# Performance work log

Hardware: AMD Instinct MI355X
Metric: run time of the kernel (lower is better)

Reference implementation:

```python
import jax, jax.numpy as jnp
import numpy as np

B, T, C, V = 8, 2048, 1024, 32000


def setup_inputs() -> dict:
    key = jax.random.key(0)
    ks = jax.random.split(key, 12)
    s = 1.0 / np.sqrt(C)
    return {
        "input_tokens": jax.random.randint(ks[0], (B, T), 0, V),
        "xx_init": jnp.zeros((B, C), jnp.float32),
        "aa_init": jnp.zeros((B, C), jnp.float32),
        "bb_init": jnp.zeros((B, C), jnp.float32),
        "pp_init": jnp.zeros((B, C), jnp.float32),  # with aa=bb=0 this is equivalent to -inf init
        "emb": jax.random.normal(ks[1], (V, C), jnp.float32) * 0.02,
        "time_mix_k": jax.random.uniform(ks[2], (C,), jnp.float32),
        "time_mix_v": jax.random.uniform(ks[3], (C,), jnp.float32),
        "time_mix_r": jax.random.uniform(ks[4], (C,), jnp.float32),
        "time_decay": jax.random.normal(ks[5], (C,), jnp.float32) * 0.1,
        "time_first": jax.random.normal(ks[6], (C,), jnp.float32) * 0.1,
        "Wk": jax.random.normal(ks[7], (C, C), jnp.float32) * s,
        "Wv": jax.random.normal(ks[8], (C, C), jnp.float32) * s,
        "Wr": jax.random.normal(ks[9], (C, C), jnp.float32) * s,
        "Wo": jax.random.normal(ks[10], (C, C), jnp.float32) * s,
    }


def _wkv_scan(k, v, aa0, bb0, pp0, w, u):
    """Numerically-stable RWKV WKV recurrence.
    k, v: [T, B, C]; aa0/bb0/pp0: [B, C]; w (decay, negative), u (bonus): [C]."""
    def step(carry, kv):
        aa, bb, pp = carry
        kt, vt = kv
        ww = u + kt
        p = jnp.maximum(pp, ww)
        e1 = jnp.exp(pp - p)
        e2 = jnp.exp(ww - p)
        wkv = (e1 * aa + e2 * vt) / (e1 * bb + e2)
        ww2 = pp + w
        p2 = jnp.maximum(ww2, kt)
        e1b = jnp.exp(ww2 - p2)
        e2b = jnp.exp(kt - p2)
        return (e1b * aa + e2b * vt, e1b * bb + e2b, p2), wkv
    (aa, bb, pp), out = jax.lax.scan(step, (aa0, bb0, pp0), (k, v))
    return out, aa, bb, pp


def _forward(input_tokens, xx_init, aa_init, bb_init, pp_init, emb,
             time_mix_k, time_mix_v, time_mix_r, time_decay, time_first,
             Wk, Wv, Wr, Wo):
    x = emb[input_tokens]                                   # [B, T, C]
    xprev = jnp.concatenate([xx_init[:, None, :], x[:, :-1]], axis=1)  # token shift
    xk = x * time_mix_k + xprev * (1.0 - time_mix_k)
    xv = x * time_mix_v + xprev * (1.0 - time_mix_v)
    xr = x * time_mix_r + xprev * (1.0 - time_mix_r)
    k = jnp.einsum("btc,dc->btd", xk, Wk)
    v = jnp.einsum("btc,dc->btd", xv, Wv)
    r = jax.nn.sigmoid(jnp.einsum("btc,dc->btd", xr, Wr))
    w = -jnp.exp(time_decay)                                # per-channel decay
    u = time_first
    wkv, _, _, _ = _wkv_scan(jnp.swapaxes(k, 0, 1), jnp.swapaxes(v, 0, 1),
                             aa_init, bb_init, pp_init, w, u)
    wkv = jnp.swapaxes(wkv, 0, 1)                           # [B, T, C]
    rwkv = jnp.einsum("btc,dc->btd", r * wkv, Wo)
    e1 = rwkv[:, -1]          # final-step state
    e2 = rwkv.mean(axis=1)    # time-averaged state
    hx = (e1 + e2) * 0.5
    return jnp.stack([hx, hx])  # (hx, cx) stacked -> [2, B, C]


def reference(input_tokens, xx_init, aa_init, bb_init, pp_init, emb,
              time_mix_k, time_mix_v, time_mix_r, time_decay, time_first,
              Wk, Wv, Wr, Wo):
    return _forward(input_tokens, xx_init, aa_init, bb_init, pp_init, emb,
                    time_mix_k, time_mix_v, time_mix_r, time_decay, time_first,
                    Wk, Wv, Wr, Wo)
```

## Files before the change

kernel.cpp:

```cpp
#include <hip/hip_runtime.h>

#define Bdim 8
#define Tdim 2048
#define Cdim 1024
#define CHUNK 128
#define NCHUNK 16
#define BC (Bdim*Cdim)

typedef float floatx4 __attribute__((ext_vector_type(4)));
typedef _Float16 half8 __attribute__((ext_vector_type(8)));
typedef _Float16 half4v __attribute__((ext_vector_type(4)));

__device__ __forceinline__ void load16(const void* g, void* l) {
    __builtin_amdgcn_global_load_lds(
        (const __attribute__((address_space(1))) void*)g,
        (__attribute__((address_space(3))) void*)l, 16, 0, 0);
}

__global__ __launch_bounds__(256) void embed_mix(const int* __restrict__ tokens,
                                                 const float* __restrict__ xx_init,
                                                 const float* __restrict__ emb,
                                                 _Float16* __restrict__ xe) {
    int row = blockIdx.x;
    int b = row / (Tdim + 1);
    int tt = row % (Tdim + 1);
    const float* src;
    if (tt == 0) src = xx_init + (size_t)b * Cdim;
    else         src = emb + (size_t)tokens[b * Tdim + tt - 1] * Cdim;
    int c0 = threadIdx.x * 4;
    float4 f = *reinterpret_cast<const float4*>(src + c0);
    half4v h;
    h[0] = (_Float16)f.x; h[1] = (_Float16)f.y; h[2] = (_Float16)f.z; h[3] = (_Float16)f.w;
    *reinterpret_cast<half4v*>(xe + (size_t)row * Cdim + c0) = h;
}

__global__ __launch_bounds__(256) void mix3(const _Float16* __restrict__ xe,
                                            const float* __restrict__ tmk,
                                            const float* __restrict__ tmv,
                                            const float* __restrict__ tmr,
                                            _Float16* __restrict__ xk,
                                            _Float16* __restrict__ xv,
                                            _Float16* __restrict__ xr) {
    int row = blockIdx.x;
    int b = row >> 11;
    int t = row & (Tdim - 1);
    const _Float16* cur = xe + ((size_t)(b * (Tdim + 1) + t + 1)) * Cdim;
    const _Float16* prv = cur - Cdim;
    int c = threadIdx.x * 4;
    half4v cu = *reinterpret_cast<const half4v*>(cur + c);
    half4v pv = *reinterpret_cast<const half4v*>(prv + c);
    float4 mk = *reinterpret_cast<const float4*>(tmk + c);
    float4 mv = *reinterpret_cast<const float4*>(tmv + c);
    float4 mr = *reinterpret_cast<const float4*>(tmr + c);
    half4v hk, hv, hr;
    float cf[4] = {(float)cu[0], (float)cu[1], (float)cu[2], (float)cu[3]};
    float pf[4] = {(float)pv[0], (float)pv[1], (float)pv[2], (float)pv[3]};
    float mkf[4] = {mk.x, mk.y, mk.z, mk.w};
    float mvf[4] = {mv.x, mv.y, mv.z, mv.w};
    float mrf[4] = {mr.x, mr.y, mr.z, mr.w};
    #pragma unroll
    for (int j = 0; j < 4; j++) {
        hk[j] = (_Float16)(mkf[j] * cf[j] + (1.0f - mkf[j]) * pf[j]);
        hv[j] = (_Float16)(mvf[j] * cf[j] + (1.0f - mvf[j]) * pf[j]);
        hr[j] = (_Float16)(mrf[j] * cf[j] + (1.0f - mrf[j]) * pf[j]);
    }
    size_t o = (size_t)row * Cdim + c;
    *reinterpret_cast<half4v*>(xk + o) = hk;
    *reinterpret_cast<half4v*>(xv + o) = hv;
    *reinterpret_cast<half4v*>(xr + o) = hr;
}

__global__ __launch_bounds__(256) void wconv(const float* __restrict__ Wk,
                                             const float* __restrict__ Wv,
                                             const float* __restrict__ Wr,
                                             _Float16* __restrict__ Wh) {
    const float* W = blockIdx.y == 0 ? Wk : (blockIdx.y == 1 ? Wv : Wr);
    _Float16* dst = Wh + (size_t)blockIdx.y * Cdim * Cdim;
    int i = (blockIdx.x * 256 + threadIdx.x) * 4;
    float4 f = *reinterpret_cast<const float4*>(W + i);
    half4v h;
    h[0] = (_Float16)f.x; h[1] = (_Float16)f.y; h[2] = (_Float16)f.z; h[3] = (_Float16)f.w;
    *reinterpret_cast<half4v*>(dst + i) = h;
}

__global__ __launch_bounds__(512, 2) void gemm_kvr(const _Float16* __restrict__ xk,
                                                   const _Float16* __restrict__ xv,
                                                   const _Float16* __restrict__ xr,
                                                   const _Float16* __restrict__ Wh,
                                                   _Float16* __restrict__ ko,
                                                   _Float16* __restrict__ vo,
                                                   _Float16* __restrict__ ro) {
    const int which = blockIdx.y;
    const _Float16* X = which == 0 ? xk : (which == 1 ? xv : xr);
    const _Float16* W = Wh + (size_t)which * Cdim * Cdim;
    _Float16* out     = which == 0 ? ko : (which == 1 ? vo : ro);

    const int lin = blockIdx.x;
    const int xcd = lin & 7;
    const int loc = lin >> 3;
    const int mt = xcd * 8 + (loc >> 2);
    const int nt = loc & 3;
    const int m0 = mt * 256;
    const int n0 = nt * 256;

    __shared__ _Float16 As[4 * 8192];
    __shared__ _Float16 Bs[4 * 8192];

    const int tid = threadIdx.x;
    const int lane = tid & 63;
    const int wave = tid >> 6;
    const int wm = (wave >> 2) * 128;
    const int wn = (wave & 3) * 64;
    const int lr = lane & 15;
    const int lk = lane >> 4;
    const int sw = (lr >> 1) & 3;

    const _Float16* Asrc = X + (size_t)m0 * Cdim;
    const _Float16* Bsrc = W + (size_t)n0 * Cdim;

    floatx4 acc[8][4] = {};

    auto stageA = [&](int kt) {
        const int p = kt & 3;
        const int k0 = kt * 32;
        #pragma unroll
        for (int i = 0; i < 2; i++) {
            int e = i * 512 + tid;
            int r = e >> 2;
            int cp = e & 3;
            int cl = cp ^ ((r >> 1) & 3);
            load16(Asrc + (size_t)r * Cdim + k0 + cl * 8, (char*)(As + p * 8192) + e * 16);
        }
    };
    auto stageB = [&](int kt) {
        const int p = kt & 3;
        const int k0 = kt * 32;
        #pragma unroll
        for (int i = 0; i < 2; i++) {
            int e = i * 512 + tid;
            int r = e >> 2;
            int cp = e & 3;
            int cl = cp ^ ((r >> 1) & 3);
            load16(Bsrc + (size_t)r * Cdim + k0 + cl * 8, (char*)(Bs + p * 8192) + e * 16);
        }
    };

    auto ktile = [&](int kt, bool st) {
        const int p = kt & 3;
        const _Float16* ap = As + p * 8192 + (wm + lr) * 32 + (lk ^ sw) * 8;
        const _Float16* bp = Bs + p * 8192 + (wn + lr) * 32 + (lk ^ sw) * 8;
        half8 af[8], bf[4];
        #pragma unroll
        for (int mi = 0; mi < 4; mi++)
            af[mi] = *reinterpret_cast<const half8*>(ap + mi * 512);
        #pragma unroll
        for (int ni = 0; ni < 4; ni++)
            bf[ni] = *reinterpret_cast<const half8*>(bp + ni * 512);
        if (st) stageA(kt + 3);
        __builtin_amdgcn_s_barrier();
        asm volatile("s_waitcnt lgkmcnt(0)" ::: "memory");
        __builtin_amdgcn_sched_barrier(0);
        __builtin_amdgcn_s_setprio(1);
        #pragma unroll
        for (int mi = 0; mi < 4; mi++)
            #pragma unroll
            for (int ni = 0; ni < 4; ni++)
                acc[mi][ni] = __builtin_amdgcn_mfma_f32_16x16x32_f16(af[mi], bf[ni], acc[mi][ni], 0, 0, 0);
        __builtin_amdgcn_s_setprio(0);
        __builtin_amdgcn_sched_barrier(0);
        __builtin_amdgcn_s_barrier();
        #pragma unroll
        for (int mi = 4; mi < 8; mi++)
            af[mi] = *reinterpret_cast<const half8*>(ap + mi * 512);
        if (st) stageB(kt + 3);
        __builtin_amdgcn_s_barrier();
        asm volatile("s_waitcnt lgkmcnt(0)" ::: "memory");
        __builtin_amdgcn_sched_barrier(0);
        __builtin_amdgcn_s_setprio(1);
        #pragma unroll
        for (int mi = 4; mi < 8; mi++)
            #pragma unroll
            for (int ni = 0; ni < 4; ni++)
                acc[mi][ni] = __builtin_amdgcn_mfma_f32_16x16x32_f16(af[mi], bf[ni], acc[mi][ni], 0, 0, 0);
        __builtin_amdgcn_s_setprio(0);
        __builtin_amdgcn_sched_barrier(0);
    };

    stageA(0); stageB(0); stageA(1); stageB(1); stageA(2); stageB(2);
    asm volatile("s_waitcnt vmcnt(8)" ::: "memory");
    __builtin_amdgcn_s_barrier();

    for (int kt = 0; kt < 29; ++kt) {
        ktile(kt, true);
        asm volatile("s_waitcnt vmcnt(8)" ::: "memory");
        __builtin_amdgcn_s_barrier();
    }
    ktile(29, false);
    asm volatile("s_waitcnt vmcnt(4)" ::: "memory");
    __builtin_amdgcn_s_barrier();
    ktile(30, false);
    asm volatile("s_waitcnt vmcnt(0)" ::: "memory");
    __builtin_amdgcn_s_barrier();
    ktile(31, false);

    #pragma unroll
    for (int mi = 0; mi < 8; mi++) {
        #pragma unroll
        for (int ni = 0; ni < 4; ni++) {
            #pragma unroll
            for (int reg = 0; reg < 4; reg++) {
                int mm = m0 + wm + mi * 16 + (lane >> 4) * 4 + reg;
                int nn = n0 + wn + ni * 16 + (lane & 15);
                float v = acc[mi][ni][reg];
                if (which == 2) v = 1.0f / (1.0f + __expf(-v));
                out[(size_t)mm * Cdim + nn] = (_Float16)v;
            }
        }
    }
}

__global__ __launch_bounds__(256) void scan_pass1(const _Float16* __restrict__ kb,
                                                  const _Float16* __restrict__ vb,
                                                  const float* __restrict__ tdecay,
                                                  float* __restrict__ tot_a,
                                                  float* __restrict__ tot_b,
                                                  float* __restrict__ tot_p) {
    int idx = blockIdx.x * 256 + threadIdx.x;
    int j = idx >> 13;
    int bc = idx & (BC - 1);
    int b = bc >> 10;
    int c = bc & (Cdim - 1);
    float w = -__expf(tdecay[c]);
    float aa = 0.0f, bb = 0.0f, pp = -1e30f;
    const _Float16* kp = kb + ((size_t)(b * Tdim + j * CHUNK)) * Cdim + c;
    const _Float16* vp = vb + ((size_t)(b * Tdim + j * CHUNK)) * Cdim + c;
    #pragma unroll 4
    for (int t = 0; t < CHUNK; t++) {
        float kt = (float)kp[(size_t)t * Cdim];
        float vt = (float)vp[(size_t)t * Cdim];
        float ww2 = pp + w;
        float p2 = fmaxf(ww2, kt);
        float e1 = __expf(ww2 - p2);
        float e2 = __expf(kt - p2);
        aa = e1 * aa + e2 * vt;
        bb = e1 * bb + e2;
        pp = p2;
    }
    tot_a[idx] = aa; tot_b[idx] = bb; tot_p[idx] = pp;
}

__global__ __launch_bounds__(256) void combine_chunks(const float* __restrict__ tot_a,
                                                      const float* __restrict__ tot_b,
                                                      const float* __restrict__ tot_p,
                                                      const float* __restrict__ aa_init,
                                                      const float* __restrict__ bb_init,
                                                      const float* __restrict__ pp_init,
                                                      const float* __restrict__ tdecay,
                                                      float* __restrict__ inc_a,
                                                      float* __restrict__ inc_b,
                                                      float* __restrict__ inc_p) {
    int idx = blockIdx.x * 256 + threadIdx.x;
    int c = idx & (Cdim - 1);
    float w = -__expf(tdecay[c]);
    float wL = w * (float)CHUNK;
    float a = aa_init[idx], b = bb_init[idx], p = pp_init[idx];
    for (int j = 0; j < NCHUNK; j++) {
        inc_a[j * BC + idx] = a;
        inc_b[j * BC + idx] = b;
        inc_p[j * BC + idx] = p;
        float ta = tot_a[j * BC + idx];
        float tb = tot_b[j * BC + idx];
        float tp = tot_p[j * BC + idx];
        float px = p + wL;
        float q = fmaxf(px, tp);
        float e1 = __expf(px - q);
        float e2 = __expf(tp - q);
        a = e1 * a + e2 * ta;
        b = e1 * b + e2 * tb;
        p = q;
    }
}

__global__ __launch_bounds__(256) void scan_pass2(const _Float16* __restrict__ kb,
                                                  const _Float16* __restrict__ vb,
                                                  const _Float16* __restrict__ rb,
                                                  const float* __restrict__ tdecay,
                                                  const float* __restrict__ tfirst,
                                                  const float* __restrict__ inc_a,
                                                  const float* __restrict__ inc_b,
                                                  const float* __restrict__ inc_p,
                                                  float* __restrict__ partial,
                                                  float* __restrict__ ylast) {
    int idx = blockIdx.x * 256 + threadIdx.x;
    int j = idx >> 13;
    int bc = idx & (BC - 1);
    int b = bc >> 10;
    int c = bc & (Cdim - 1);
    float w = -__expf(tdecay[c]);
    float u = tfirst[c];
    float aa = inc_a[idx], bb = inc_b[idx], pp = inc_p[idx];
    const size_t base = ((size_t)(b * Tdim + j * CHUNK)) * Cdim + c;
    const _Float16* kp = kb + base;
    const _Float16* vp = vb + base;
    const _Float16* rp = rb + base;
    float sum = 0.0f, ylv = 0.0f;
    #pragma unroll 4
    for (int t = 0; t < CHUNK; t++) {
        float kt = (float)kp[(size_t)t * Cdim];
        float vt = (float)vp[(size_t)t * Cdim];
        float rt = (float)rp[(size_t)t * Cdim];
        float ww = u + kt;
        float p = fmaxf(pp, ww);
        float e1 = __expf(pp - p);
        float e2 = __expf(ww - p);
        float wkv = (e1 * aa + e2 * vt) / (e1 * bb + e2);
        float y = rt * wkv;
        sum += y;
        ylv = y;
        float ww2 = pp + w;
        float p2 = fmaxf(ww2, kt);
        float e1b = __expf(ww2 - p2);
        float e2b = __expf(kt - p2);
        aa = e1b * aa + e2b * vt;
        bb = e1b * bb + e2b;
        pp = p2;
    }
    partial[idx] = sum;
    if (j == NCHUNK - 1) ylast[bc] = ylv;
}

__global__ __launch_bounds__(256) void reduce_z(const float* __restrict__ partial,
                                                const float* __restrict__ ylast,
                                                float* __restrict__ z) {
    int idx = blockIdx.x * 256 + threadIdx.x;
    float s = 0.0f;
    for (int j = 0; j < NCHUNK; j++) s += partial[j * BC + idx];
    z[idx] = 0.5f * (ylast[idx] + s * (1.0f / (float)Tdim));
}

__global__ __launch_bounds__(256) void final_out(const float* __restrict__ z,
                                                 const float* __restrict__ Wo,
                                                 float* __restrict__ out) {
    int gw = (blockIdx.x * 256 + threadIdx.x) >> 6;
    int lane = threadIdx.x & 63;
    int b = gw >> 10;
    int d = gw & (Cdim - 1);
    const float* zr = z + (size_t)b * Cdim;
    const float* wr = Wo + (size_t)d * Cdim;
    float acc = 0.0f;
    #pragma unroll
    for (int i = lane; i < Cdim; i += 64) acc += zr[i] * wr[i];
    #pragma unroll
    for (int off = 32; off > 0; off >>= 1) acc += __shfl_down(acc, off);
    if (lane == 0) {
        out[(size_t)b * Cdim + d] = acc;
        out[(size_t)BC + (size_t)b * Cdim + d] = acc;
    }
}

extern "C" void kernel_launch(void* const* d_in, const int* in_sizes, int n_in,
                              void* d_out, int out_size, void* d_ws, size_t ws_size,
                              hipStream_t stream) {
    const int*   tokens  = (const int*)d_in[0];
    const float* xx_init = (const float*)d_in[1];
    const float* aa_init = (const float*)d_in[2];
    const float* bb_init = (const float*)d_in[3];
    const float* pp_init = (const float*)d_in[4];
    const float* emb     = (const float*)d_in[5];
    const float* tmk     = (const float*)d_in[6];
    const float* tmv     = (const float*)d_in[7];
    const float* tmr     = (const float*)d_in[8];
    const float* tdecay  = (const float*)d_in[9];
    const float* tfirst  = (const float*)d_in[10];
    const float* Wk      = (const float*)d_in[11];
    const float* Wv      = (const float*)d_in[12];
    const float* Wr      = (const float*)d_in[13];
    const float* Wo      = (const float*)d_in[14];
    float* out = (float*)d_out;

    char* ws = (char*)d_ws;
    size_t off = 0;
    auto alloc = [&](size_t bytes) -> void* {
        void* p = ws + off;
        off += (bytes + 255) & ~(size_t)255;
        return p;
    };
    _Float16* xe = (_Float16*)alloc((size_t)Bdim * (Tdim + 1) * Cdim * 2);
    _Float16* xkb = (_Float16*)alloc((size_t)Bdim * Tdim * Cdim * 2);
    _Float16* xvb = (_Float16*)alloc((size_t)Bdim * Tdim * Cdim * 2);
    _Float16* xrb = (_Float16*)alloc((size_t)Bdim * Tdim * Cdim * 2);
    _Float16* kb = xe;
    _Float16* vb = (_Float16*)alloc((size_t)Bdim * Tdim * Cdim * 2);
    _Float16* rb = (_Float16*)alloc((size_t)Bdim * Tdim * Cdim * 2);
    _Float16* Wh = (_Float16*)alloc((size_t)3 * Cdim * Cdim * 2);
    float* tot_a = (float*)alloc((size_t)NCHUNK * BC * 4);
    float* tot_b = (float*)alloc((size_t)NCHUNK * BC * 4);
    float* tot_p = (float*)alloc((size_t)NCHUNK * BC * 4);
    float* inc_a = (float*)alloc((size_t)NCHUNK * BC * 4);
    float* inc_b = (float*)alloc((size_t)NCHUNK * BC * 4);
    float* inc_p = (float*)alloc((size_t)NCHUNK * BC * 4);
    float* partial = (float*)alloc((size_t)NCHUNK * BC * 4);
    float* ylast   = (float*)alloc((size_t)BC * 4);
    float* zbuf    = (float*)alloc((size_t)BC * 4);

    embed_mix<<<Bdim * (Tdim + 1), 256, 0, stream>>>(tokens, xx_init, emb, xe);
    mix3<<<Bdim * Tdim, 256, 0, stream>>>(xe, tmk, tmv, tmr, xkb, xvb, xrb);
    wconv<<<dim3(1024, 3), 256, 0, stream>>>(Wk, Wv, Wr, Wh);
    gemm_kvr<<<dim3(256, 3), 512, 0, stream>>>(xkb, xvb, xrb, Wh, kb, vb, rb);
    scan_pass1<<<(NCHUNK * BC) / 256, 256, 0, stream>>>(kb, vb, tdecay, tot_a, tot_b, tot_p);
    combine_chunks<<<BC / 256, 256, 0, stream>>>(tot_a, tot_b, tot_p, aa_init, bb_init, pp_init,
                                                 tdecay, inc_a, inc_b, inc_p);
    scan_pass2<<<(NCHUNK * BC) / 256, 256, 0, stream>>>(kb, vb, rb, tdecay, tfirst,
                                                        inc_a, inc_b, inc_p, partial, ylast);
    reduce_z<<<BC / 256, 256, 0, stream>>>(partial, ylast, zbuf);
    final_out<<<(BC / 4), 256, 0, stream>>>(zbuf, Wo, out);
}
```

Baseline: 410.3 us.

## Fuse embedding gather into token-shift mix and halve scan chunk length

Merges the embedding gather and the time-mix kernel so each row reads the current and previous fp32 embedding rows directly, removing the intermediate fp16 buffer and one launch. Halves the chunk length of the chunked WKV scan (doubling the chunk count) to raise parallelism in the two scan passes, at the cost of larger chunk-state buffers and a longer serial combine loop. Adds unroll pragmas to the combine and reduce loops and gives the k output its own buffer instead of aliasing the removed one.

```diff
diff --git a/kernel.cpp b/kernel.cpp
--- a/kernel.cpp
+++ b/kernel.cpp
@@ -3,8 +3,8 @@
 #define Bdim 8
 #define Tdim 2048
 #define Cdim 1024
-#define CHUNK 128
-#define NCHUNK 16
+#define CHUNK 64
+#define NCHUNK 32
 #define BC (Bdim*Cdim)
 
 typedef float floatx4 __attribute__((ext_vector_type(4)));
@@ -17,47 +17,33 @@
         (__attribute__((address_space(3))) void*)l, 16, 0, 0);
 }
 
-__global__ __launch_bounds__(256) void embed_mix(const int* __restrict__ tokens,
+__global__ __launch_bounds__(256) void fused_mix(const int* __restrict__ tokens,
                                                  const float* __restrict__ xx_init,
                                                  const float* __restrict__ emb,
-                                                 _Float16* __restrict__ xe) {
-    int row = blockIdx.x;
-    int b = row / (Tdim + 1);
-    int tt = row % (Tdim + 1);
-    const float* src;
-    if (tt == 0) src = xx_init + (size_t)b * Cdim;
-    else         src = emb + (size_t)tokens[b * Tdim + tt - 1] * Cdim;
-    int c0 = threadIdx.x * 4;
-    float4 f = *reinterpret_cast<const float4*>(src + c0);
-    half4v h;
-    h[0] = (_Float16)f.x; h[1] = (_Float16)f.y; h[2] = (_Float16)f.z; h[3] = (_Float16)f.w;
-    *reinterpret_cast<half4v*>(xe + (size_t)row * Cdim + c0) = h;
-}
-
-__global__ __launch_bounds__(256) void mix3(const _Float16* __restrict__ xe,
-                                            const float* __restrict__ tmk,
-                                            const float* __restrict__ tmv,
-                                            const float* __restrict__ tmr,
-                                            _Float16* __restrict__ xk,
-                                            _Float16* __restrict__ xv,
-                                            _Float16* __restrict__ xr) {
+                                                 const float* __restrict__ tmk,
+                                                 const float* __restrict__ tmv,
+                                                 const float* __restrict__ tmr,
+                                                 _Float16* __restrict__ xk,
+                                                 _Float16* __restrict__ xv,
+                                                 _Float16* __restrict__ xr) {
     int row = blockIdx.x;
     int b = row >> 11;
     int t = row & (Tdim - 1);
-    const _Float16* cur = xe + ((size_t)(b * (Tdim + 1) + t + 1)) * Cdim;
-    const _Float16* prv = cur - Cdim;
+    const float* cur = emb + (size_t)tokens[row] * Cdim;
+    const float* prv = (t == 0) ? (xx_init + (size_t)b * Cdim)
+                                : (emb + (size_t)tokens[row - 1] * Cdim);
     int c = threadIdx.x * 4;
-    half4v cu = *reinterpret_cast<const half4v*>(cur + c);
-    half4v pv = *reinterpret_cast<const half4v*>(prv + c);
+    float4 cu = *reinterpret_cast<const float4*>(cur + c);
+    float4 pv = *reinterpret_cast<const float4*>(prv + c);
     float4 mk = *reinterpret_cast<const float4*>(tmk + c);
     float4 mv = *reinterpret_cast<const float4*>(tmv + c);
     float4 mr = *reinterpret_cast<const float4*>(tmr + c);
-    half4v hk, hv, hr;
-    float cf[4] = {(float)cu[0], (float)cu[1], (float)cu[2], (float)cu[3]};
-    float pf[4] = {(float)pv[0], (float)pv[1], (float)pv[2], (float)pv[3]};
+    float cf[4] = {cu.x, cu.y, cu.z, cu.w};
+    float pf[4] = {pv.x, pv.y, pv.z, pv.w};
     float mkf[4] = {mk.x, mk.y, mk.z, mk.w};
     float mvf[4] = {mv.x, mv.y, mv.z, mv.w};
     float mrf[4] = {mr.x, mr.y, mr.z, mr.w};
+    half4v hk, hv, hr;
     #pragma unroll
     for (int j = 0; j < 4; j++) {
         hk[j] = (_Float16)(mkf[j] * cf[j] + (1.0f - mkf[j]) * pf[j]);
@@ -264,6 +250,7 @@
     float w = -__expf(tdecay[c]);
     float wL = w * (float)CHUNK;
     float a = aa_init[idx], b = bb_init[idx], p = pp_init[idx];
+    #pragma unroll 4
     for (int j = 0; j < NCHUNK; j++) {
         inc_a[j * BC + idx] = a;
         inc_b[j * BC + idx] = b;
@@ -334,6 +321,7 @@
                                                 float* __restrict__ z) {
     int idx = blockIdx.x * 256 + threadIdx.x;
     float s = 0.0f;
+    #pragma unroll 4
     for (int j = 0; j < NCHUNK; j++) s += partial[j * BC + idx];
     z[idx] = 0.5f * (ylast[idx] + s * (1.0f / (float)Tdim));
 }
@@ -385,13 +373,12 @@
         off += (bytes + 255) & ~(size_t)255;
         return p;
     };
-    _Float16* xe = (_Float16*)alloc((size_t)Bdim * (Tdim + 1) * Cdim * 2);
     _Float16* xkb = (_Float16*)alloc((size_t)Bdim * Tdim * Cdim * 2);
     _Float16* xvb = (_Float16*)alloc((size_t)Bdim * Tdim * Cdim * 2);
     _Float16* xrb = (_Float16*)alloc((size_t)Bdim * Tdim * Cdim * 2);
-    _Float16* kb = xe;
-    _Float16* vb = (_Float16*)alloc((size_t)Bdim * Tdim * Cdim * 2);
-    _Float16* rb = (_Float16*)alloc((size_t)Bdim * Tdim * Cdim * 2);
+    _Float16* kb  = (_Float16*)alloc((size_t)Bdim * Tdim * Cdim * 2);
+    _Float16* vb  = (_Float16*)alloc((size_t)Bdim * Tdim * Cdim * 2);
+    _Float16* rb  = (_Float16*)alloc((size_t)Bdim * Tdim * Cdim * 2);
     _Float16* Wh = (_Float16*)alloc((size_t)3 * Cdim * Cdim * 2);
     float* tot_a = (float*)alloc((size_t)NCHUNK * BC * 4);
     float* tot_b = (float*)alloc((size_t)NCHUNK * BC * 4);
@@ -403,8 +390,8 @@
     float* ylast   = (float*)alloc((size_t)BC * 4);
     float* zbuf    = (float*)alloc((size_t)BC * 4);
 
-    embed_mix<<<Bdim * (Tdim + 1), 256, 0, stream>>>(tokens, xx_init, emb, xe);
-    mix3<<<Bdim * Tdim, 256, 0, stream>>>(xe, tmk, tmv, tmr, xkb, xvb, xrb);
+    fused_mix<<<Bdim * Tdim, 256, 0, stream>>>(tokens, xx_init, emb, tmk, tmv, tmr,
+                                               xkb, xvb, xrb);
     wconv<<<dim3(1024, 3), 256, 0, stream>>>(Wk, Wv, Wr, Wh);
     gemm_kvr<<<dim3(256, 3), 512, 0, stream>>>(xkb, xvb, xrb, Wh, kb, vb, rb);
     scan_pass1<<<(NCHUNK * BC) / 256, 256, 0, stream>>>(kb, vb, tdecay, tot_a, tot_b, tot_p);
```

After: 409.9 us (median of 2 runs). No clear change (-0.1%).
